# Kernel tuning notes

Measured on AMD Instinct MI355X. Metric: run time of the kernel, lower is better.

The kernel has to match this reference:

```python
import jax, jax.numpy as jnp
import numpy as np

NUM_HEADS = 12
HIDDEN = 768
HEAD = HIDDEN // NUM_HEADS
SCALE = HIDDEN ** (-0.5)  # NB: module scales by hidden_dim**-0.5, not head_size**-0.5


def setup_inputs() -> dict:
    key = jax.random.key(0)
    ks = jax.random.split(key, 8)
    B, N = 16, 512
    std = HIDDEN ** (-0.5)
    return {
        "x": jax.random.normal(ks[0], (B, N, HIDDEN), dtype=jnp.float32),
        "encoding_bias": jax.random.normal(ks[1], (B, N, N), dtype=jnp.float32),
        "Wq": jax.random.normal(ks[2], (HIDDEN, HIDDEN), dtype=jnp.float32) * std,
        "Wk": jax.random.normal(ks[3], (HIDDEN, HIDDEN), dtype=jnp.float32) * std,
        "Wv": jax.random.normal(ks[4], (HIDDEN, HIDDEN), dtype=jnp.float32) * std,
        "bv": jax.random.normal(ks[5], (HIDDEN,), dtype=jnp.float32) * 0.01,
        "Wo": jax.random.normal(ks[6], (HIDDEN, HIDDEN), dtype=jnp.float32) * std,
        "bo": jax.random.normal(ks[7], (HIDDEN,), dtype=jnp.float32) * 0.01,
    }


def reference(x, encoding_bias, Wq, Wk, Wv, bv, Wo, bo):
    B, N, _ = x.shape
    # torch nn.Linear: y = x @ W.T (+ b)
    q = (x @ Wq.T).reshape(B, N, NUM_HEADS, HEAD)
    k = (x @ Wk.T).reshape(B, N, NUM_HEADS, HEAD)
    v = (x @ Wv.T + bv).reshape(B, N, NUM_HEADS, HEAD)
    # scores: [B, H, N, N] with additive graph bias broadcast over heads
    a = jnp.einsum("bnhd,bmhd->bhnm", q, k) * SCALE + encoding_bias[:, None, :, :]
    # data-dependent pad mask: rows whose scores are identically zero
    pad_mask = jnp.all(a == 0, axis=-1)  # [B, H, N]
    a = jnp.where(pad_mask[..., None], -jnp.inf, a)
    a = jax.nn.softmax(a, axis=-1)
    a = jnp.nan_to_num(a)  # all -inf rows -> NaN -> 0
    o = jnp.einsum("bhnm,bmhd->bnhd", a, v).reshape(B, N, HIDDEN)
    # dropout is identity in eval mode
    return o @ Wo.T + bo
```

## Files before the change

### kernel.cpp

```cpp
#include <hip/hip_runtime.h>
#include <stdint.h>

typedef unsigned short u16;
typedef unsigned int u32;
typedef __bf16 bf16x8 __attribute__((ext_vector_type(8)));
typedef float f32x4 __attribute__((ext_vector_type(4)));

#define NH 12
#define HD 64
#define SEQ 512
#define BATCH 16
#define HID 768
#define SCALE_Q 0.03608439182435161f

__device__ __forceinline__ u16 f2bf(float f) {
    u32 u = __builtin_bit_cast(u32, f);
    u32 r = (u + 0x7FFFu + ((u >> 16) & 1u)) >> 16;
    return (u16)r;
}
__device__ __forceinline__ float bf2f(u16 h) {
    return __builtin_bit_cast(float, (u32)h << 16);
}

__device__ __forceinline__ void gl2lds16(const u16* g, u16* lds_base) {
    __builtin_amdgcn_global_load_lds(
        (const __attribute__((address_space(1))) u32*)g,
        (__attribute__((address_space(3))) u32*)lds_base, 16, 0, 0);
}

#define NXB 6144
#define NEB 4096
#define NWB 576
__global__ void cvt_all(const float* __restrict__ x, const float* __restrict__ eb,
                        const float* __restrict__ w0, const float* __restrict__ w1,
                        const float* __restrict__ w2, const float* __restrict__ w3,
                        u16* __restrict__ dst) {
    int b = blockIdx.x;
    const float* s; int sb;
    if (b < NXB) { s = x; sb = 0; }
    else if (b < NXB + NEB) { s = eb; sb = NXB; }
    else if (b < NXB + NEB + NWB) { s = w0; sb = NXB + NEB; }
    else if (b < NXB + NEB + 2 * NWB) { s = w1; sb = NXB + NEB + NWB; }
    else if (b < NXB + NEB + 3 * NWB) { s = w2; sb = NXB + NEB + 2 * NWB; }
    else { s = w3; sb = NXB + NEB + 3 * NWB; }
    int li = (b - sb) * 1024 + threadIdx.x * 4;
    float4 v = *(const float4*)(s + li);
    ushort4 o;
    o.x = f2bf(v.x); o.y = f2bf(v.y); o.z = f2bf(v.z); o.w = f2bf(v.w);
    *(ushort4*)(dst + (size_t)b * 1024 + threadIdx.x * 4) = o;
}

__device__ __forceinline__ void stage_gemm(
    const u16* __restrict__ Ag, const u16* __restrict__ Bg, int k0,
    u16* As, u16* Bs, int r0, int q0, int r1, int q1, int w)
{
    gl2lds16(Ag + (size_t)r0 * HID + k0 + q0, As + w * 512);
    gl2lds16(Ag + (size_t)r1 * HID + k0 + q1, As + 2048 + w * 512);
    gl2lds16(Bg + (size_t)r0 * HID + k0 + q0, Bs + w * 512);
    gl2lds16(Bg + (size_t)r1 * HID + k0 + q1, Bs + 2048 + w * 512);
}

__device__ __forceinline__ void gemm_mainloop(
    const u16* __restrict__ Ag, const u16* __restrict__ Bg,
    u16 (*As)[128 * 32], u16 (*Bs)[128 * 32], f32x4 (&acc)[4][4])
{
    const int tid = threadIdx.x;
    const int l = tid & 63, w = tid >> 6;
    const int wm = w & 1, wn = w >> 1;
    const int lr = l & 15, lg = l >> 4;

    const int c0 = tid, c1 = tid + 256;
    const int r0 = c0 >> 2, q0 = (c0 & 3) * 8;
    const int r1 = c1 >> 2, q1 = (c1 & 3) * 8;

    stage_gemm(Ag, Bg, 0, As[0], Bs[0], r0, q0, r1, q1, w);

    for (int i = 0; i < 24; i++) {
        const int cur = i & 1;
        __syncthreads();
        if (i < 23)
            stage_gemm(Ag, Bg, (i + 1) * 32, As[cur ^ 1], Bs[cur ^ 1], r0, q0, r1, q1, w);

        bf16x8 af[4], bfr[4];
#pragma unroll
        for (int mi = 0; mi < 4; mi++)
            af[mi] = *(const bf16x8*)(As[cur] + (wm * 64 + mi * 16 + lr) * 32 + lg * 8);
#pragma unroll
        for (int ni = 0; ni < 4; ni++)
            bfr[ni] = *(const bf16x8*)(Bs[cur] + (wn * 64 + ni * 16 + lr) * 32 + lg * 8);
#pragma unroll
        for (int mi = 0; mi < 4; mi++)
#pragma unroll
            for (int ni = 0; ni < 4; ni++)
                acc[mi][ni] = __builtin_amdgcn_mfma_f32_16x16x32_bf16(af[mi], bfr[ni], acc[mi][ni], 0, 0, 0);
    }
}

__global__ __launch_bounds__(256, 4) void gemm_qkv(
    const u16* __restrict__ xb, const u16* __restrict__ wq,
    const u16* __restrict__ wk, const u16* __restrict__ wv,
    const float* __restrict__ bv,
    u16* __restrict__ qtb, u16* __restrict__ kb, u16* __restrict__ vtb)
{
    __shared__ __align__(16) u16 As[2][128 * 32];
    __shared__ __align__(16) u16 Bs[2][128 * 32];
    const int tid = threadIdx.x;
    const int l = tid & 63, w = tid >> 6;
    const int wm = w & 1, wn = w >> 1;
    const int lr = l & 15, lg = l >> 4;
    const int mt = blockIdx.x, nt = blockIdx.y, z = blockIdx.z;

    const u16* Bw = (z == 0) ? wq : (z == 1) ? wk : wv;
    const u16* Ag = xb + (size_t)(mt * 128) * HID;
    const u16* Bg = Bw + (size_t)(nt * 128) * HID;

    f32x4 acc[4][4] = {};
    gemm_mainloop(Ag, Bg, As, Bs, acc);

    const float sc = (z == 0) ? SCALE_Q : 1.0f;
#pragma unroll
    for (int mi = 0; mi < 4; mi++) {
#pragma unroll
        for (int ni = 0; ni < 4; ni++) {
            const int jg = nt * 128 + wn * 64 + ni * 16 + lr;
            const int h = jg >> 6, d = jg & 63;
            const int i0 = mt * 128 + wm * 64 + mi * 16 + lg * 4;
            const int b = i0 >> 9, n0 = i0 & 511;
            if (z == 1) {
#pragma unroll
                for (int r = 0; r < 4; r++)
                    kb[((size_t)(b * NH + h) * SEQ + n0 + r) * HD + d] = f2bf(acc[mi][ni][r]);
            } else {
                float bb = (z == 2) ? bv[jg] : 0.0f;
                ushort4 pk;
                pk.x = f2bf(fmaf(acc[mi][ni][0], sc, bb));
                pk.y = f2bf(fmaf(acc[mi][ni][1], sc, bb));
                pk.z = f2bf(fmaf(acc[mi][ni][2], sc, bb));
                pk.w = f2bf(fmaf(acc[mi][ni][3], sc, bb));
                u16* O = (z == 0) ? qtb : vtb;
                *(ushort4*)(O + ((size_t)(b * NH + h) * HD + d) * SEQ + n0) = pk;
            }
        }
    }
}

__global__ __launch_bounds__(256, 4) void gemm_out(
    const u16* __restrict__ A, const u16* __restrict__ wo,
    const float* __restrict__ bo, float* __restrict__ Cout)
{
    __shared__ __align__(16) u16 As[2][128 * 32];
    __shared__ __align__(16) u16 Bs[2][128 * 32];
    const int tid = threadIdx.x;
    const int l = tid & 63, w = tid >> 6;
    const int wm = w & 1, wn = w >> 1;
    const int lr = l & 15, lg = l >> 4;
    const int mt = blockIdx.x, nt = blockIdx.y;

    const u16* Ag = A + (size_t)(mt * 128) * HID;
    const u16* Bg = wo + (size_t)(nt * 128) * HID;

    f32x4 acc[4][4] = {};
    gemm_mainloop(Ag, Bg, As, Bs, acc);

#pragma unroll
    for (int mi = 0; mi < 4; mi++) {
#pragma unroll
        for (int ni = 0; ni < 4; ni++) {
            const int jg = nt * 128 + wn * 64 + ni * 16 + lr;
            float bb = bo[jg];
#pragma unroll
            for (int r = 0; r < 4; r++) {
                int ig = mt * 128 + wm * 64 + mi * 16 + lg * 4 + r;
                Cout[(size_t)ig * HID + jg] = acc[mi][ni][r] + bb;
            }
        }
    }
}

__device__ __forceinline__ void stage_kv(
    const u16* __restrict__ Kg, const u16* __restrict__ Vg, int mt0,
    u16* Ksb, u16* Vsb, int kr0, int kc0, int kr1, int kc1, int w)
{
    gl2lds16(Kg + (size_t)(mt0 + kr0) * HD + kc0 * 8, Ksb + w * 512);
    gl2lds16(Kg + (size_t)(mt0 + kr1) * HD + kc1 * 8, Ksb + 2048 + w * 512);
    gl2lds16(Vg + (size_t)kr0 * SEQ + mt0 + kc0 * 8, Vsb + w * 512);
    gl2lds16(Vg + (size_t)kr1 * SEQ + mt0 + kc1 * 8, Vsb + 2048 + w * 512);
}

__global__ __launch_bounds__(256, 4) void attn_kernel(
    const u16* __restrict__ qtb, const u16* __restrict__ kb, const u16* __restrict__ vtb,
    const u16* __restrict__ ebb, u16* __restrict__ ob)
{
    __shared__ __align__(16) u16 Ks[2][64 * 64];
    __shared__ __align__(16) u16 Vs[2][64 * 64];
    __shared__ __align__(16) u16 Ps[4][16 * 64];

    const int tid = threadIdx.x;
    const int l = tid & 63, w = tid >> 6;
    const int lr = l & 15, lg = l >> 4;
    const int h = blockIdx.x, qt = blockIdx.y, b = blockIdx.z;
    const int bh = b * NH + h;
    const int qrow0 = qt * 64 + w * 16;

    const u16* Kg = kb + (size_t)bh * SEQ * HD;
    const u16* Vg = vtb + (size_t)bh * HD * SEQ;
    const u16* Eg = ebb + ((size_t)b * SEQ + qrow0 + lg * 4) * SEQ;

    const int p0 = tid, p1 = tid + 256;
    const int kr0 = p0 >> 3, kc0 = (p0 & 7) ^ (kr0 & 7);
    const int kr1 = p1 >> 3, kc1 = (p1 & 7) ^ (kr1 & 7);

    stage_kv(Kg, Vg, 0, Ks[0], Vs[0], kr0, kc0, kr1, kc1, w);

    const u16* Qg = qtb + (size_t)bh * HD * SEQ + qrow0 + lr;
    bf16x8 qf0, qf1;
#pragma unroll
    for (int j = 0; j < 8; j++) {
        qf0[j] = __builtin_bit_cast(__bf16, Qg[(size_t)(lg * 8 + j) * SEQ]);
        qf1[j] = __builtin_bit_cast(__bf16, Qg[(size_t)(lg * 8 + j + 32) * SEQ]);
    }

    bf16x8 ones;
#pragma unroll
    for (int j = 0; j < 8; j++) ones[j] = __builtin_bit_cast(__bf16, (u16)0x3F80);

    f32x4 oacc[4] = {};
    f32x4 lacc = {};
    float amax[4] = {0.f, 0.f, 0.f, 0.f};

    for (int t = 0; t < 8; t++) {
        const int cur = t & 1;
        const int mt0 = t * 64;
        __syncthreads();

        u16 bl[4][4];
#pragma unroll
        for (int mi = 0; mi < 4; mi++)
#pragma unroll
            for (int r = 0; r < 4; r++)
                bl[mi][r] = Eg[(size_t)r * SEQ + mt0 + mi * 16 + lr];

        if (t < 7)
            stage_kv(Kg, Vg, mt0 + 64, Ks[cur ^ 1], Vs[cur ^ 1], kr0, kc0, kr1, kc1, w);

        float sm[4][4];
#pragma unroll
        for (int mi = 0; mi < 4; mi++) {
            const int row = mi * 16 + lr;
            bf16x8 kf0 = *(const bf16x8*)(Ks[cur] + row * 64 + ((lg ^ (row & 7)) * 8));
            bf16x8 kf1 = *(const bf16x8*)(Ks[cur] + row * 64 + (((4 + lg) ^ (row & 7)) * 8));
            f32x4 s;
#pragma unroll
            for (int r = 0; r < 4; r++) s[r] = bf2f(bl[mi][r]);
            s = __builtin_amdgcn_mfma_f32_16x16x32_bf16(qf0, kf0, s, 0, 0, 0);
            s = __builtin_amdgcn_mfma_f32_16x16x32_bf16(qf1, kf1, s, 0, 0, 0);
#pragma unroll
            for (int r = 0; r < 4; r++) {
                float sv = s[r];
                amax[r] = fmaxf(amax[r], fabsf(sv));
                sm[mi][r] = __expf(sv);
            }
        }

        u16* Pw = Ps[w];
#pragma unroll
        for (int mi = 0; mi < 4; mi++)
#pragma unroll
            for (int r = 0; r < 4; r++) {
                const int q = lg * 4 + r;
                const int chunk = mi * 2 + (lr >> 3);
                Pw[q * 64 + ((chunk ^ (q & 7)) * 8) + (lr & 7)] = f2bf(sm[mi][r]);
            }

#pragma unroll
        for (int ks = 0; ks < 2; ks++) {
            bf16x8 pf = *(const bf16x8*)(Pw + lr * 64 + (((ks * 4 + lg) ^ (lr & 7)) * 8));
#pragma unroll
            for (int di = 0; di < 4; di++) {
                const int row = di * 16 + lr;
                bf16x8 vf = *(const bf16x8*)(Vs[cur] + row * 64 + (((ks * 4 + lg) ^ (row & 7)) * 8));
                oacc[di] = __builtin_amdgcn_mfma_f32_16x16x32_bf16(pf, vf, oacc[di], 0, 0, 0);
            }
            lacc = __builtin_amdgcn_mfma_f32_16x16x32_bf16(pf, ones, lacc, 0, 0, 0);
        }
    }

#pragma unroll
    for (int r = 0; r < 4; r++) {
        float am = amax[r];
        am = fmaxf(am, __shfl_xor(am, 1));
        am = fmaxf(am, __shfl_xor(am, 2));
        am = fmaxf(am, __shfl_xor(am, 4));
        am = fmaxf(am, __shfl_xor(am, 8));
        float inv = (am > 0.f) ? (1.0f / lacc[r]) : 0.0f;
        int n = qrow0 + lg * 4 + r;
        u16* orow = ob + ((size_t)b * SEQ + n) * HID + h * HD;
#pragma unroll
        for (int di = 0; di < 4; di++)
            orow[di * 16 + lr] = f2bf(oacc[di][r] * inv);
    }
}

extern "C" void kernel_launch(void* const* d_in, const int* in_sizes, int n_in,
                              void* d_out, int out_size, void* d_ws, size_t ws_size,
                              hipStream_t stream) {
    (void)in_sizes; (void)n_in; (void)out_size; (void)ws_size;
    const float* x  = (const float*)d_in[0];
    const float* eb = (const float*)d_in[1];
    const float* Wq = (const float*)d_in[2];
    const float* Wk = (const float*)d_in[3];
    const float* Wv = (const float*)d_in[4];
    const float* bv = (const float*)d_in[5];
    const float* Wo = (const float*)d_in[6];
    const float* bo = (const float*)d_in[7];
    float* out = (float*)d_out;

    const int NX = BATCH * SEQ * HID;
    const int NW = HID * HID;
    const int NE = BATCH * SEQ * SEQ;
    u16* ws   = (u16*)d_ws;
    u16* xb   = ws;
    u16* ebb  = xb + NX;
    u16* wqb  = ebb + NE;
    u16* wkb  = wqb + NW;
    u16* wvb  = wkb + NW;
    u16* wob  = wvb + NW;
    u16* qtb  = wob + NW;
    u16* kb   = qtb + NX;
    u16* vtb  = kb + NX;
    u16* obuf = vtb + NX;

    cvt_all<<<NXB + NEB + 4 * NWB, 256, 0, stream>>>(x, eb, Wq, Wk, Wv, Wo, ws);

    gemm_qkv<<<dim3(64, 6, 3), 256, 0, stream>>>(xb, wqb, wkb, wvb, bv, qtb, kb, vtb);

    attn_kernel<<<dim3(NH, 8, BATCH), 256, 0, stream>>>(qtb, kb, vtb, ebb, obuf);

    gemm_out<<<dim3(64, 6), 256, 0, stream>>>(obuf, wob, bo, out);
}
```

Baseline: 208.8 us.

## Remap block indices for XCD-aware locality and reorganize GEMM LDS layout

After: 249.1 us. 1.19x slower.

```diff
diff --git a/kernel.cpp b/kernel.cpp
--- a/kernel.cpp
+++ b/kernel.cpp
@@ -52,12 +52,12 @@
 
 __device__ __forceinline__ void stage_gemm(
     const u16* __restrict__ Ag, const u16* __restrict__ Bg, int k0,
-    u16* As, u16* Bs, int r0, int q0, int r1, int q1, int w)
-{
-    gl2lds16(Ag + (size_t)r0 * HID + k0 + q0, As + w * 512);
-    gl2lds16(Ag + (size_t)r1 * HID + k0 + q1, As + 2048 + w * 512);
-    gl2lds16(Bg + (size_t)r0 * HID + k0 + q0, Bs + w * 512);
-    gl2lds16(Bg + (size_t)r1 * HID + k0 + q1, Bs + 2048 + w * 512);
+    u16* As, u16* Bs, int r, int q8, int w)
+{
+    gl2lds16(Ag + (size_t)r * HID + k0 + q8,      As + w * 512);
+    gl2lds16(Ag + (size_t)r * HID + k0 + q8 + 16, As + 2048 + w * 512);
+    gl2lds16(Bg + (size_t)r * HID + k0 + q8,      Bs + w * 512);
+    gl2lds16(Bg + (size_t)r * HID + k0 + q8 + 16, Bs + 2048 + w * 512);
 }
 
 __device__ __forceinline__ void gemm_mainloop(
@@ -69,25 +69,23 @@
     const int wm = w & 1, wn = w >> 1;
     const int lr = l & 15, lg = l >> 4;
 
-    const int c0 = tid, c1 = tid + 256;
-    const int r0 = c0 >> 2, q0 = (c0 & 3) * 8;
-    const int r1 = c1 >> 2, q1 = (c1 & 3) * 8;
-
-    stage_gemm(Ag, Bg, 0, As[0], Bs[0], r0, q0, r1, q1, w);
+    const int r = tid & 127, q8 = (tid >> 7) * 8;
+
+    stage_gemm(Ag, Bg, 0, As[0], Bs[0], r, q8, w);
 
     for (int i = 0; i < 24; i++) {
         const int cur = i & 1;
         __syncthreads();
         if (i < 23)
-            stage_gemm(Ag, Bg, (i + 1) * 32, As[cur ^ 1], Bs[cur ^ 1], r0, q0, r1, q1, w);
+            stage_gemm(Ag, Bg, (i + 1) * 32, As[cur ^ 1], Bs[cur ^ 1], r, q8, w);
 
         bf16x8 af[4], bfr[4];
 #pragma unroll
         for (int mi = 0; mi < 4; mi++)
-            af[mi] = *(const bf16x8*)(As[cur] + (wm * 64 + mi * 16 + lr) * 32 + lg * 8);
+            af[mi] = *(const bf16x8*)(As[cur] + lg * 1024 + (wm * 64 + mi * 16 + lr) * 8);
 #pragma unroll
         for (int ni = 0; ni < 4; ni++)
-            bfr[ni] = *(const bf16x8*)(Bs[cur] + (wn * 64 + ni * 16 + lr) * 32 + lg * 8);
+            bfr[ni] = *(const bf16x8*)(Bs[cur] + lg * 1024 + (wn * 64 + ni * 16 + lr) * 8);
 #pragma unroll
         for (int mi = 0; mi < 4; mi++)
 #pragma unroll
@@ -108,7 +106,11 @@
     const int l = tid & 63, w = tid >> 6;
     const int wm = w & 1, wn = w >> 1;
     const int lr = l & 15, lg = l >> 4;
-    const int mt = blockIdx.x, nt = blockIdx.y, z = blockIdx.z;
+
+    const int L = blockIdx.x;
+    const int g = L & 7, rest = L >> 3;
+    const int ntz = rest % 18, mt = (rest / 18) * 8 + g;
+    const int z = ntz / 6, nt = ntz % 6;
 
     const u16* Bw = (z == 0) ? wq : (z == 1) ? wk : wv;
     const u16* Ag = xb + (size_t)(mt * 128) * HID;
@@ -128,8 +130,8 @@
             const int b = i0 >> 9, n0 = i0 & 511;
             if (z == 1) {
 #pragma unroll
-                for (int r = 0; r < 4; r++)
-                    kb[((size_t)(b * NH + h) * SEQ + n0 + r) * HD + d] = f2bf(acc[mi][ni][r]);
+                for (int r2 = 0; r2 < 4; r2++)
+                    kb[((size_t)(b * NH + h) * SEQ + n0 + r2) * HD + d] = f2bf(acc[mi][ni][r2]);
             } else {
                 float bb = (z == 2) ? bv[jg] : 0.0f;
                 ushort4 pk;
@@ -154,7 +156,10 @@
     const int l = tid & 63, w = tid >> 6;
     const int wm = w & 1, wn = w >> 1;
     const int lr = l & 15, lg = l >> 4;
-    const int mt = blockIdx.x, nt = blockIdx.y;
+
+    const int L = blockIdx.x;
+    const int g = L & 7, rest = L >> 3;
+    const int nt = rest % 6, mt = (rest / 6) * 8 + g;
 
     const u16* Ag = A + (size_t)(mt * 128) * HID;
     const u16* Bg = wo + (size_t)(nt * 128) * HID;
@@ -169,9 +174,9 @@
             const int jg = nt * 128 + wn * 64 + ni * 16 + lr;
             float bb = bo[jg];
 #pragma unroll
-            for (int r = 0; r < 4; r++) {
-                int ig = mt * 128 + wm * 64 + mi * 16 + lg * 4 + r;
-                Cout[(size_t)ig * HID + jg] = acc[mi][ni][r] + bb;
+            for (int r2 = 0; r2 < 4; r2++) {
+                int ig = mt * 128 + wm * 64 + mi * 16 + lg * 4 + r2;
+                Cout[(size_t)ig * HID + jg] = acc[mi][ni][r2] + bb;
             }
         }
     }
@@ -198,8 +203,11 @@
     const int tid = threadIdx.x;
     const int l = tid & 63, w = tid >> 6;
     const int lr = l & 15, lg = l >> 4;
-    const int h = blockIdx.x, qt = blockIdx.y, b = blockIdx.z;
-    const int bh = b * NH + h;
+
+    const int L = blockIdx.x;
+    const int g = L & 7, rest = L >> 3;
+    const int qt = rest & 7, bh = (rest >> 3) * 8 + g;
+    const int b = bh / NH, h = bh % NH;
     const int qrow0 = qt * 64 + w * 16;
 
     const u16* Kg = kb + (size_t)bh * SEQ * HD;
@@ -332,9 +340,9 @@
 
     cvt_all<<<NXB + NEB + 4 * NWB, 256, 0, stream>>>(x, eb, Wq, Wk, Wv, Wo, ws);
 
-    gemm_qkv<<<dim3(64, 6, 3), 256, 0, stream>>>(xb, wqb, wkb, wvb, bv, qtb, kb, vtb);
-
-    attn_kernel<<<dim3(NH, 8, BATCH), 256, 0, stream>>>(qtb, kb, vtb, ebb, obuf);
-
-    gemm_out<<<dim3(64, 6), 256, 0, stream>>>(obuf, wob, bo, out);
-}
+    gemm_qkv<<<1152, 256, 0, stream>>>(xb, wqb, wkb, wvb, bv, qtb, kb, vtb);
+
+    attn_kernel<<<1536, 256, 0, stream>>>(qtb, kb, vtb, ebb, obuf);
+
+    gemm_out<<<384, 256, 0, stream>>>(obuf, wob, bo, out);
+}
```

## Replace LDS staging with direct global fragment loads in GEMMs and attention

Applied to the files above, without the earlier changes.

Result: slower. 356.8 us (+70.9%).

```diff
diff --git a/kernel.cpp b/kernel.cpp
--- a/kernel.cpp
+++ b/kernel.cpp
@@ -20,12 +20,6 @@
 }
 __device__ __forceinline__ float bf2f(u16 h) {
     return __builtin_bit_cast(float, (u32)h << 16);
-}
-
-__device__ __forceinline__ void gl2lds16(const u16* g, u16* lds_base) {
-    __builtin_amdgcn_global_load_lds(
-        (const __attribute__((address_space(1))) u32*)g,
-        (__attribute__((address_space(3))) u32*)lds_base, 16, 0, 0);
 }
 
 #define NXB 6144
@@ -50,60 +44,51 @@
     *(ushort4*)(dst + (size_t)b * 1024 + threadIdx.x * 4) = o;
 }
 
-__device__ __forceinline__ void stage_gemm(
-    const u16* __restrict__ Ag, const u16* __restrict__ Bg, int k0,
-    u16* As, u16* Bs, int r0, int q0, int r1, int q1, int w)
-{
-    gl2lds16(Ag + (size_t)r0 * HID + k0 + q0, As + w * 512);
-    gl2lds16(Ag + (size_t)r1 * HID + k0 + q1, As + 2048 + w * 512);
-    gl2lds16(Bg + (size_t)r0 * HID + k0 + q0, Bs + w * 512);
-    gl2lds16(Bg + (size_t)r1 * HID + k0 + q1, Bs + 2048 + w * 512);
+__device__ __forceinline__ void load_frags(
+    const u16* __restrict__ A0, const u16* __restrict__ B0, int koff,
+    bf16x8 (&af)[4], bf16x8 (&bfr)[4])
+{
+#pragma unroll
+    for (int mi = 0; mi < 4; mi++)
+        af[mi] = *(const bf16x8*)(A0 + (size_t)mi * 16 * HID + koff);
+#pragma unroll
+    for (int ni = 0; ni < 4; ni++)
+        bfr[ni] = *(const bf16x8*)(B0 + (size_t)ni * 16 * HID + koff);
 }
 
 __device__ __forceinline__ void gemm_mainloop(
-    const u16* __restrict__ Ag, const u16* __restrict__ Bg,
-    u16 (*As)[128 * 32], u16 (*Bs)[128 * 32], f32x4 (&acc)[4][4])
+    const u16* __restrict__ Ag, const u16* __restrict__ Bg, f32x4 (&acc)[4][4])
 {
     const int tid = threadIdx.x;
     const int l = tid & 63, w = tid >> 6;
     const int wm = w & 1, wn = w >> 1;
     const int lr = l & 15, lg = l >> 4;
 
-    const int c0 = tid, c1 = tid + 256;
-    const int r0 = c0 >> 2, q0 = (c0 & 3) * 8;
-    const int r1 = c1 >> 2, q1 = (c1 & 3) * 8;
-
-    stage_gemm(Ag, Bg, 0, As[0], Bs[0], r0, q0, r1, q1, w);
+    const u16* A0 = Ag + (size_t)(wm * 64 + lr) * HID + lg * 8;
+    const u16* B0 = Bg + (size_t)(wn * 64 + lr) * HID + lg * 8;
+
+    bf16x8 af[4], bfr[4], afn[4], bfn[4];
+    load_frags(A0, B0, 0, af, bfr);
 
     for (int i = 0; i < 24; i++) {
-        const int cur = i & 1;
-        __syncthreads();
         if (i < 23)
-            stage_gemm(Ag, Bg, (i + 1) * 32, As[cur ^ 1], Bs[cur ^ 1], r0, q0, r1, q1, w);
-
-        bf16x8 af[4], bfr[4];
-#pragma unroll
-        for (int mi = 0; mi < 4; mi++)
-            af[mi] = *(const bf16x8*)(As[cur] + (wm * 64 + mi * 16 + lr) * 32 + lg * 8);
-#pragma unroll
-        for (int ni = 0; ni < 4; ni++)
-            bfr[ni] = *(const bf16x8*)(Bs[cur] + (wn * 64 + ni * 16 + lr) * 32 + lg * 8);
+            load_frags(A0, B0, (i + 1) * 32, afn, bfn);
 #pragma unroll
         for (int mi = 0; mi < 4; mi++)
 #pragma unroll
             for (int ni = 0; ni < 4; ni++)
                 acc[mi][ni] = __builtin_amdgcn_mfma_f32_16x16x32_bf16(af[mi], bfr[ni], acc[mi][ni], 0, 0, 0);
-    }
-}
-
-__global__ __launch_bounds__(256, 4) void gemm_qkv(
+#pragma unroll
+        for (int j = 0; j < 4; j++) { af[j] = afn[j]; bfr[j] = bfn[j]; }
+    }
+}
+
+__global__ __launch_bounds__(256, 3) void gemm_qkv(
     const u16* __restrict__ xb, const u16* __restrict__ wq,
     const u16* __restrict__ wk, const u16* __restrict__ wv,
     const float* __restrict__ bv,
     u16* __restrict__ qtb, u16* __restrict__ kb, u16* __restrict__ vtb)
 {
-    __shared__ __align__(16) u16 As[2][128 * 32];
-    __shared__ __align__(16) u16 Bs[2][128 * 32];
     const int tid = threadIdx.x;
     const int l = tid & 63, w = tid >> 6;
     const int wm = w & 1, wn = w >> 1;
@@ -115,7 +100,7 @@
     const u16* Bg = Bw + (size_t)(nt * 128) * HID;
 
     f32x4 acc[4][4] = {};
-    gemm_mainloop(Ag, Bg, As, Bs, acc);
+    gemm_mainloop(Ag, Bg, acc);
 
     const float sc = (z == 0) ? SCALE_Q : 1.0f;
 #pragma unroll
@@ -128,8 +113,8 @@
             const int b = i0 >> 9, n0 = i0 & 511;
             if (z == 1) {
 #pragma unroll
-                for (int r = 0; r < 4; r++)
-                    kb[((size_t)(b * NH + h) * SEQ + n0 + r) * HD + d] = f2bf(acc[mi][ni][r]);
+                for (int r2 = 0; r2 < 4; r2++)
+                    kb[((size_t)(b * NH + h) * SEQ + n0 + r2) * HD + d] = f2bf(acc[mi][ni][r2]);
             } else {
                 float bb = (z == 2) ? bv[jg] : 0.0f;
                 ushort4 pk;
@@ -144,12 +129,10 @@
     }
 }
 
-__global__ __launch_bounds__(256, 4) void gemm_out(
+__global__ __launch_bounds__(256, 3) void gemm_out(
     const u16* __restrict__ A, const u16* __restrict__ wo,
     const float* __restrict__ bo, float* __restrict__ Cout)
 {
-    __shared__ __align__(16) u16 As[2][128 * 32];
-    __shared__ __align__(16) u16 Bs[2][128 * 32];
     const int tid = threadIdx.x;
     const int l = tid & 63, w = tid >> 6;
     const int wm = w & 1, wn = w >> 1;
@@ -160,7 +143,7 @@
     const u16* Bg = wo + (size_t)(nt * 128) * HID;
 
     f32x4 acc[4][4] = {};
-    gemm_mainloop(Ag, Bg, As, Bs, acc);
+    gemm_mainloop(Ag, Bg, acc);
 
 #pragma unroll
     for (int mi = 0; mi < 4; mi++) {
@@ -169,30 +152,18 @@
             const int jg = nt * 128 + wn * 64 + ni * 16 + lr;
             float bb = bo[jg];
 #pragma unroll
-            for (int r = 0; r < 4; r++) {
-                int ig = mt * 128 + wm * 64 + mi * 16 + lg * 4 + r;
-                Cout[(size_t)ig * HID + jg] = acc[mi][ni][r] + bb;
-            }
-        }
-    }
-}
-
-__device__ __forceinline__ void stage_kv(
-    const u16* __restrict__ Kg, const u16* __restrict__ Vg, int mt0,
-    u16* Ksb, u16* Vsb, int kr0, int kc0, int kr1, int kc1, int w)
-{
-    gl2lds16(Kg + (size_t)(mt0 + kr0) * HD + kc0 * 8, Ksb + w * 512);
-    gl2lds16(Kg + (size_t)(mt0 + kr1) * HD + kc1 * 8, Ksb + 2048 + w * 512);
-    gl2lds16(Vg + (size_t)kr0 * SEQ + mt0 + kc0 * 8, Vsb + w * 512);
-    gl2lds16(Vg + (size_t)kr1 * SEQ + mt0 + kc1 * 8, Vsb + 2048 + w * 512);
+            for (int r2 = 0; r2 < 4; r2++) {
+                int ig = mt * 128 + wm * 64 + mi * 16 + lg * 4 + r2;
+                Cout[(size_t)ig * HID + jg] = acc[mi][ni][r2] + bb;
+            }
+        }
+    }
 }
 
 __global__ __launch_bounds__(256, 4) void attn_kernel(
     const u16* __restrict__ qtb, const u16* __restrict__ kb, const u16* __restrict__ vtb,
     const u16* __restrict__ ebb, u16* __restrict__ ob)
 {
-    __shared__ __align__(16) u16 Ks[2][64 * 64];
-    __shared__ __align__(16) u16 Vs[2][64 * 64];
     __shared__ __align__(16) u16 Ps[4][16 * 64];
 
     const int tid = threadIdx.x;
@@ -206,12 +177,6 @@
     const u16* Vg = vtb + (size_t)bh * HD * SEQ;
     const u16* Eg = ebb + ((size_t)b * SEQ + qrow0 + lg * 4) * SEQ;
 
-    const int p0 = tid, p1 = tid + 256;
-    const int kr0 = p0 >> 3, kc0 = (p0 & 7) ^ (kr0 & 7);
-    const int kr1 = p1 >> 3, kc1 = (p1 & 7) ^ (kr1 & 7);
-
-    stage_kv(Kg, Vg, 0, Ks[0], Vs[0], kr0, kc0, kr1, kc1, w);
-
     const u16* Qg = qtb + (size_t)bh * HD * SEQ + qrow0 + lr;
     bf16x8 qf0, qf1;
 #pragma unroll
@@ -229,9 +194,7 @@
     float amax[4] = {0.f, 0.f, 0.f, 0.f};
 
     for (int t = 0; t < 8; t++) {
-        const int cur = t & 1;
         const int mt0 = t * 64;
-        __syncthreads();
 
         u16 bl[4][4];
 #pragma unroll
@@ -240,15 +203,12 @@
             for (int r = 0; r < 4; r++)
                 bl[mi][r] = Eg[(size_t)r * SEQ + mt0 + mi * 16 + lr];
 
-        if (t < 7)
-            stage_kv(Kg, Vg, mt0 + 64, Ks[cur ^ 1], Vs[cur ^ 1], kr0, kc0, kr1, kc1, w);
-
         float sm[4][4];
 #pragma unroll
         for (int mi = 0; mi < 4; mi++) {
-            const int row = mi * 16 + lr;
-            bf16x8 kf0 = *(const bf16x8*)(Ks[cur] + row * 64 + ((lg ^ (row & 7)) * 8));
-            bf16x8 kf1 = *(const bf16x8*)(Ks[cur] + row * 64 + (((4 + lg) ^ (row & 7)) * 8));
+            const u16* Kr = Kg + (size_t)(mt0 + mi * 16 + lr) * HD + lg * 8;
+            bf16x8 kf0 = *(const bf16x8*)(Kr);
+            bf16x8 kf1 = *(const bf16x8*)(Kr + 32);
             f32x4 s;
 #pragma unroll
             for (int r = 0; r < 4; r++) s[r] = bf2f(bl[mi][r]);
@@ -277,8 +237,7 @@
             bf16x8 pf = *(const bf16x8*)(Pw + lr * 64 + (((ks * 4 + lg) ^ (lr & 7)) * 8));
 #pragma unroll
             for (int di = 0; di < 4; di++) {
-                const int row = di * 16 + lr;
-                bf16x8 vf = *(const bf16x8*)(Vs[cur] + row * 64 + (((ks * 4 + lg) ^ (row & 7)) * 8));
+                bf16x8 vf = *(const bf16x8*)(Vg + (size_t)(di * 16 + lr) * SEQ + mt0 + ks * 32 + lg * 8);
                 oacc[di] = __builtin_amdgcn_mfma_f32_16x16x32_bf16(pf, vf, oacc[di], 0, 0, 0);
             }
             lacc = __builtin_amdgcn_mfma_f32_16x16x32_bf16(pf, ones, lacc, 0, 0, 0);
```
